# Kernel optimization log

Hardware: AMD Instinct MI355X
Metric: run time of the kernel (lower is better)

Reference implementation:

```python
import jax, jax.numpy as jnp
import numpy as np

NS_STEPS = 10
NS_A, NS_B, NS_C = 3.4445, -4.7750, 2.0315  # standard quintic Newton-Schulz coefficients
EPS = 1e-7

def orthogonalize(w):
    """Newton-Schulz iteration producing a (near-)orthogonal matrix from w."""
    din, dout = w.shape
    transpose = din > dout  # iterate on the wide orientation so X @ X.T is small
    x = w.T if transpose else w
    x = x / (jnp.linalg.norm(x) + EPS)  # spectral norm <= frobenius norm -> contraction

    def body(x, _):
        a = x @ x.T                      # (m, m) Gram matrix
        bmat = NS_B * a + NS_C * (a @ a)
        x = NS_A * x + bmat @ x
        return x, None

    x, _ = jax.lax.scan(body, x, None, length=NS_STEPS)
    return x.T if transpose else x


def setup_inputs() -> dict:
    key = jax.random.key(0)
    k1, k2, k3 = jax.random.split(key, 3)
    B, DIN, DOUT = 16384, 2048, 2048
    x = jax.random.normal(k1, (B, DIN), dtype=jnp.float32)
    w = jax.random.normal(k2, (DIN, DOUT), dtype=jnp.float32)
    b = jax.random.normal(k3, (DOUT,), dtype=jnp.float32) * 0.02
    return {"x": x, "w": w, "b": b}


def reference(x, w, b):
    w_orth = orthogonalize(w)
    return x @ w_orth + b
```

## Files before the change

### kernel.cpp

```cpp
#include <hip/hip_runtime.h>
#include <stdint.h>

typedef unsigned short u16;
typedef _Float16 half_t;
typedef __attribute__((ext_vector_type(4))) float f32x4;
typedef __attribute__((ext_vector_type(8))) _Float16 f16x8;

#define NS_A 3.4445f
#define NS_B -4.7750f
#define NS_C 2.0315f

#define SX      64.0f
#define INV_SX  (1.0f / 64.0f)
#define INV_SA  (1.0f / 4096.0f)

typedef const __attribute__((address_space(1))) void* as1_cvp;
typedef __attribute__((address_space(3))) void* as3_vp;
#define GLOAD_LDS16(gp, lp) \
    __builtin_amdgcn_global_load_lds((as1_cvp)(const void*)(gp), (as3_vp)(void*)(lp), 16, 0, 0)

template <int N> __device__ __forceinline__ void vmwait() {
    if constexpr (N == 0)       asm volatile("s_waitcnt vmcnt(0)" ::: "memory");
    else if constexpr (N == 4)  asm volatile("s_waitcnt vmcnt(4)" ::: "memory");
    else if constexpr (N == 6)  asm volatile("s_waitcnt vmcnt(6)" ::: "memory");
    else if constexpr (N == 8)  asm volatile("s_waitcnt vmcnt(8)" ::: "memory");
    else if constexpr (N == 12) asm volatile("s_waitcnt vmcnt(12)" ::: "memory");
    else static_assert(N == 0, "unsupported vmcnt");
}

template <int MODE>
__global__ __launch_bounds__(256, 2) void gemm_ns(
    const half_t* __restrict__ A, const half_t* __restrict__ B,
    const half_t* __restrict__ aux,
    void* __restrict__ outp, half_t* __restrict__ outpT,
    int M, int N, int K)
{
    __shared__ half_t As[3][64 * 64];
    __shared__ half_t Bs[3][128 * 64];
    const int tid  = threadIdx.x;
    const int wid  = tid >> 6;
    const int lane = tid & 63;
    const int wr = wid >> 1, wc = wid & 1;

    const int xcd = blockIdx.x & 7;
    const int ii  = blockIdx.x >> 3;
    const int brow = ((xcd & 1) * 16 + (ii >> 2)) * 64;
    const int bcol = ((xcd >> 1) * 4 + (ii & 3)) * 128;

    f32x4 acc[2][4] = {};

    const int r0   = tid >> 3;
    const int csrc = ((tid & 7) ^ ((tid >> 3) & 7)) * 8;
    const half_t* gA = A + (size_t)(brow + r0) * K + csrc;
    const half_t* gB = B + (size_t)(bcol + r0) * K + csrc;

    auto stage = [&](int slot, int kt) {
#pragma unroll
        for (int j = 0; j < 2; ++j)
            GLOAD_LDS16(gA + (size_t)(j * 32) * K + kt, &As[slot][(j * 256 + wid * 64) * 8]);
#pragma unroll
        for (int j = 0; j < 4; ++j)
            GLOAD_LDS16(gB + (size_t)(j * 32) * K + kt, &Bs[slot][(j * 256 + wid * 64) * 8]);
    };

    f16x8 af[2][2], bf[4][2];
    auto reads = [&](int slot) {
#pragma unroll
        for (int m = 0; m < 2; ++m) {
            const int row = wr * 32 + m * 16 + (lane & 15);
#pragma unroll
            for (int kk = 0; kk < 2; ++kk) {
                const int cc = (kk * 4 + (lane >> 4)) ^ (row & 7);
                af[m][kk] = *(const f16x8*)&As[slot][row * 64 + cc * 8];
            }
        }
#pragma unroll
        for (int n = 0; n < 4; ++n) {
            const int row = wc * 64 + n * 16 + (lane & 15);
#pragma unroll
            for (int kk = 0; kk < 2; ++kk) {
                const int cc = (kk * 4 + (lane >> 4)) ^ (row & 7);
                bf[n][kk] = *(const f16x8*)&Bs[slot][row * 64 + cc * 8];
            }
        }
    };
    auto mfma = [&]() {
        __builtin_amdgcn_s_setprio(1);
#pragma unroll
        for (int kk = 0; kk < 2; ++kk)
#pragma unroll
            for (int m = 0; m < 2; ++m)
#pragma unroll
                for (int n = 0; n < 4; ++n)
                    acc[m][n] = __builtin_amdgcn_mfma_f32_16x16x32_f16(af[m][kk], bf[n][kk], acc[m][n], 0, 0, 0);
        __builtin_amdgcn_s_setprio(0);
    };

    const int nsteps = K / 64;
    stage(0, 0);
    stage(1, 64);
    vmwait<6>();
    __builtin_amdgcn_s_barrier();

    int s = 0;
    for (; s < nsteps - 2; ++s) {
        reads(s % 3);
        stage((s + 2) % 3, (s + 2) * 64);
        vmwait<6>();
        __builtin_amdgcn_s_barrier();
        mfma();
        __builtin_amdgcn_s_barrier();
    }
    reads(s % 3);
    vmwait<0>();
    __builtin_amdgcn_s_barrier();
    mfma();
    __builtin_amdgcn_s_barrier();
    ++s;
    reads(s % 3);
    mfma();

#pragma unroll
    for (int m = 0; m < 2; ++m) {
#pragma unroll
        for (int n = 0; n < 4; ++n) {
            const int row0 = brow + wr * 32 + m * 16 + (lane >> 4) * 4;
            const int col  = bcol + wc * 64 + n * 16 + (lane & 15);
#pragma unroll
            for (int r = 0; r < 4; ++r) {
                const size_t idx = (size_t)(row0 + r) * N + col;
                const float v = acc[m][n][r];
                if (MODE == 0) {
                    ((half_t*)outp)[idx] = (half_t)v;
                } else if (MODE == 1) {
                    ((half_t*)outp)[idx] = (half_t)(NS_B * (float)aux[idx] + NS_C * v * INV_SA);
                } else {
                    const half_t o = (half_t)(NS_A * (float)aux[idx] + v * INV_SA);
                    ((half_t*)outp)[idx] = o;
                    if (outpT) outpT[(size_t)col * M + row0 + r] = o;
                }
            }
        }
    }
}

__global__ __launch_bounds__(512, 2) void gemm_fin(
    const half_t* __restrict__ A, const half_t* __restrict__ B,
    const float* __restrict__ bias, float* __restrict__ out,
    int M, int N, int K)
{
    __shared__ half_t As[4][256 * 32];
    __shared__ half_t Bs[4][256 * 32];
    const int tid  = threadIdx.x;
    const int wid  = tid >> 6;
    const int lane = tid & 63;
    const int wm = wid >> 2;
    const int wn = wid & 3;

    int bid = blockIdx.x;
    const int cpx = gridDim.x >> 3;
    bid = (bid & 7) * cpx + (bid >> 3);
    const int nbx  = N >> 8;
    const int brow = (bid / nbx) << 8;
    const int bcol = (bid % nbx) << 8;

    f32x4 acc[8][4] = {};

    const int r0   = tid >> 2;
    const int csrc = ((tid & 3) ^ ((tid >> 3) & 3)) * 8;
    const half_t* gA = A + (size_t)(brow + r0) * K + csrc;
    const half_t* gB = B + (size_t)(bcol + r0) * K + csrc;

    auto stage = [&](int slot, int kt) {
#pragma unroll
        for (int j = 0; j < 2; ++j)
            GLOAD_LDS16(gA + (size_t)(j * 128) * K + kt, &As[slot][(j * 512 + wid * 64) * 8]);
#pragma unroll
        for (int j = 0; j < 2; ++j)
            GLOAD_LDS16(gB + (size_t)(j * 128) * K + kt, &Bs[slot][(j * 512 + wid * 64) * 8]);
    };
    auto compute = [&](int slot) {
        f16x8 af[8], bf[4];
#pragma unroll
        for (int fr = 0; fr < 8; ++fr) {
            const int row = wm * 128 + fr * 16 + (lane & 15);
            af[fr] = *(const f16x8*)&As[slot][row * 32 + (((lane >> 4) ^ ((row >> 1) & 3)) * 8)];
        }
#pragma unroll
        for (int fc = 0; fc < 4; ++fc) {
            const int row = wn * 64 + fc * 16 + (lane & 15);
            bf[fc] = *(const f16x8*)&Bs[slot][row * 32 + (((lane >> 4) ^ ((row >> 1) & 3)) * 8)];
        }
        __builtin_amdgcn_s_setprio(1);
#pragma unroll
        for (int fr = 0; fr < 8; ++fr)
#pragma unroll
            for (int fc = 0; fc < 4; ++fc)
                acc[fr][fc] = __builtin_amdgcn_mfma_f32_16x16x32_f16(af[fr], bf[fc], acc[fr][fc], 0, 0, 0);
        __builtin_amdgcn_s_setprio(0);
    };

    stage(0, 0);
    stage(1, 32);
    stage(2, 64);
    int kt_next = 96;

#define RSTEP(SLOT, DOSTAGE, VMN) \
    do { \
        if (DOSTAGE) { stage((SLOT + 3) & 3, kt_next); kt_next += 32; } \
        vmwait<VMN>(); \
        __builtin_amdgcn_s_barrier(); \
        compute(SLOT); \
        __builtin_amdgcn_s_barrier(); \
    } while (0)

    const int nouter = ((K >> 5) - 4) >> 2;
    for (int tt = 0; tt < nouter; ++tt) {
        RSTEP(0, true, 12);
        RSTEP(1, true, 12);
        RSTEP(2, true, 12);
        RSTEP(3, true, 12);
    }
    RSTEP(0, true, 12);
    RSTEP(1, false, 8);
    RSTEP(2, false, 4);
    RSTEP(3, false, 0);
#undef RSTEP

#pragma unroll
    for (int fr = 0; fr < 8; ++fr) {
#pragma unroll
        for (int fc = 0; fc < 4; ++fc) {
            const int row0 = brow + wm * 128 + fr * 16 + (lane >> 4) * 4;
            const int col  = bcol + wn * 64 + fc * 16 + (lane & 15);
            const float bv = bias[col];
#pragma unroll
            for (int r = 0; r < 4; ++r)
                out[(size_t)(row0 + r) * N + col] = acc[fr][fc][r] * INV_SX + bv;
        }
    }
}

__global__ __launch_bounds__(256) void k_sumsq(const float* __restrict__ w,
                                               float* __restrict__ part, int n) {
    __shared__ float s[256];
    const int per  = n / 1024;
    const int base = blockIdx.x * per;
    float acc = 0.f;
    for (int i = threadIdx.x; i < per; i += 256) {
        float v = w[base + i];
        acc += v * v;
    }
    s[threadIdx.x] = acc;
    __syncthreads();
    for (int k = 128; k > 0; k >>= 1) {
        if (threadIdx.x < k) s[threadIdx.x] += s[threadIdx.x + k];
        __syncthreads();
    }
    if (threadIdx.x == 0) part[blockIdx.x] = s[0];
}

__global__ __launch_bounds__(256) void k_scalefin(const float* __restrict__ part,
                                                  float* __restrict__ scale) {
    __shared__ float s[256];
    float acc = 0.f;
    for (int i = threadIdx.x; i < 1024; i += 256) acc += part[i];
    s[threadIdx.x] = acc;
    __syncthreads();
    for (int k = 128; k > 0; k >>= 1) {
        if (threadIdx.x < k) s[threadIdx.x] += s[threadIdx.x + k];
        __syncthreads();
    }
    if (threadIdx.x == 0) scale[0] = SX / (sqrtf(s[0]) + 1e-7f);
}

__global__ __launch_bounds__(256) void k_scale_f16(const float* __restrict__ w,
                                                   const float* __restrict__ scale,
                                                   half_t* __restrict__ o, int n) {
    const int i = (blockIdx.x * 256 + threadIdx.x) * 4;
    if (i < n) {
        const float sc = scale[0];
        float4 v = *(const float4*)(w + i);
        o[i + 0] = (half_t)(v.x * sc);
        o[i + 1] = (half_t)(v.y * sc);
        o[i + 2] = (half_t)(v.z * sc);
        o[i + 3] = (half_t)(v.w * sc);
    }
}

__global__ __launch_bounds__(256) void k_cast_f16(const float* __restrict__ w,
                                                  half_t* __restrict__ o, int n) {
    const int i = (blockIdx.x * 256 + threadIdx.x) * 4;
    if (i < n) {
        float4 v = *(const float4*)(w + i);
        o[i + 0] = (half_t)v.x;
        o[i + 1] = (half_t)v.y;
        o[i + 2] = (half_t)v.z;
        o[i + 3] = (half_t)v.w;
    }
}

__global__ __launch_bounds__(256) void k_transpose(const u16* __restrict__ in,
                                                   u16* __restrict__ out, int n) {
    __shared__ u16 tile[64][65];
    const int bx = blockIdx.x * 64, by = blockIdx.y * 64;
    const int tx = threadIdx.x & 63, ty = threadIdx.x >> 6;
    for (int i = ty; i < 64; i += 4) tile[i][tx] = in[(size_t)(by + i) * n + bx + tx];
    __syncthreads();
    for (int i = ty; i < 64; i += 4) out[(size_t)(bx + i) * n + by + tx] = tile[tx][i];
}

extern "C" void kernel_launch(void* const* d_in, const int* in_sizes, int n_in,
                              void* d_out, int out_size, void* d_ws, size_t ws_size,
                              hipStream_t stream) {
    const float* x = (const float*)d_in[0];
    const float* w = (const float*)d_in[1];
    const float* b = (const float*)d_in[2];
    float* out = (float*)d_out;

    const int D  = 2048;
    const int Bm = in_sizes[0] / D;
    const int WN = D * D;
    const int XN = Bm * D;

    const size_t matB = (size_t)WN * 2;
    const bool pingpong = ws_size >= 8192 + 6 * matB + (size_t)XN * 2;

    char* ws = (char*)d_ws;
    float* part  = (float*)ws;
    float* scale = part + 1024;
    half_t* xb0  = (half_t*)(ws + 8192);
    half_t* xb1  = xb0 + WN;
    half_t* xbTa = xb1 + WN;
    half_t* xbTb = pingpong ? (xbTa + WN) : xbTa;
    half_t* amat = xbTb + WN;
    half_t* bmat = amat + WN;
    half_t* xinb = bmat + WN;

    k_sumsq<<<1024, 256, 0, stream>>>(w, part, WN);
    k_scalefin<<<1, 256, 0, stream>>>(part, scale);
    k_scale_f16<<<WN / 4 / 256, 256, 0, stream>>>(w, scale, xb0, WN);

    k_cast_f16<<<XN / 4 / 256, 256, 0, stream>>>(x, xinb, XN);

    const dim3 tgrid(D / 64, D / 64);
    k_transpose<<<tgrid, 256, 0, stream>>>((const u16*)xb0, (u16*)xbTa, D);

    const int ns_grid = (D / 64) * (D / 128);

    half_t* cur = xb0;
    half_t* nxt = xb1;
    half_t* Tr  = xbTa;
    half_t* Tw  = xbTb;
    for (int it = 0; it < 10; ++it) {
        gemm_ns<0><<<ns_grid, 256, 0, stream>>>(cur, cur, nullptr, amat, nullptr, D, D, D);
        gemm_ns<1><<<ns_grid, 256, 0, stream>>>(amat, amat, amat, bmat, nullptr, D, D, D);
        if (pingpong) {
            gemm_ns<2><<<ns_grid, 256, 0, stream>>>(bmat, Tr, cur, nxt, Tw, D, D, D);
            half_t* tt = Tr; Tr = Tw; Tw = tt;
        } else {
            gemm_ns<2><<<ns_grid, 256, 0, stream>>>(bmat, Tr, cur, nxt, nullptr, D, D, D);
            k_transpose<<<tgrid, 256, 0, stream>>>((const u16*)nxt, (u16*)Tr, D);
        }
        half_t* t = cur; cur = nxt; nxt = t;
    }

    const int fin_grid = (Bm / 256) * (D / 256);
    gemm_fin<<<fin_grid, 512, 0, stream>>>(xinb, Tr, b, out, Bm, D, D);
}
```

Before: 951.6 us.

## Exploit symmetry of Gram matrices with triangular-tile GEMM kernel

Result: no change. 963.9 us (+1.3%).

```diff
diff --git a/kernel.cpp b/kernel.cpp
--- a/kernel.cpp
+++ b/kernel.cpp
@@ -144,6 +144,121 @@
     }
 }
 
+template <int MODE>
+__global__ __launch_bounds__(256, 3) void gemm_sym(
+    const half_t* __restrict__ A, const half_t* __restrict__ aux,
+    half_t* __restrict__ outp, int N, int K)
+{
+    __shared__ half_t As[3][64 * 64];
+    __shared__ half_t Bs[3][64 * 64];
+    const int tid  = threadIdx.x;
+    const int wid  = tid >> 6;
+    const int lane = tid & 63;
+    const int wr = wid >> 1, wc = wid & 1;
+
+    const int bid = (blockIdx.x & 7) * 66 + (blockIdx.x >> 3);
+    int bi = (int)(32.5f - sqrtf(32.5f * 32.5f - 2.0f * (float)bid));
+    bi = bi < 0 ? 0 : (bi > 31 ? 31 : bi);
+    while (bi < 31 && (32 * (bi + 1) - ((bi + 1) * bi) / 2) <= bid) ++bi;
+    while (bi > 0 && (32 * bi - (bi * (bi - 1)) / 2) > bid) --bi;
+    const int bj = bi + (bid - (32 * bi - (bi * (bi - 1)) / 2));
+
+    const int brow = bi * 64;
+    const int bcol = bj * 64;
+
+    f32x4 acc[2][2] = {};
+
+    const int r0   = tid >> 3;
+    const int csrc = ((tid & 7) ^ ((tid >> 3) & 7)) * 8;
+    const half_t* gA = A + (size_t)(brow + r0) * K + csrc;
+    const half_t* gB = A + (size_t)(bcol + r0) * K + csrc;
+
+    auto stage = [&](int slot, int kt) {
+#pragma unroll
+        for (int j = 0; j < 2; ++j) {
+            GLOAD_LDS16(gA + (size_t)(j * 32) * K + kt, &As[slot][(j * 256 + wid * 64) * 8]);
+            GLOAD_LDS16(gB + (size_t)(j * 32) * K + kt, &Bs[slot][(j * 256 + wid * 64) * 8]);
+        }
+    };
+
+    f16x8 af[2][2], bf[2][2];
+    auto reads = [&](int slot) {
+#pragma unroll
+        for (int m = 0; m < 2; ++m) {
+            const int row = wr * 32 + m * 16 + (lane & 15);
+#pragma unroll
+            for (int kk = 0; kk < 2; ++kk) {
+                const int cc = (kk * 4 + (lane >> 4)) ^ (row & 7);
+                af[m][kk] = *(const f16x8*)&As[slot][row * 64 + cc * 8];
+            }
+        }
+#pragma unroll
+        for (int n = 0; n < 2; ++n) {
+            const int row = wc * 32 + n * 16 + (lane & 15);
+#pragma unroll
+            for (int kk = 0; kk < 2; ++kk) {
+                const int cc = (kk * 4 + (lane >> 4)) ^ (row & 7);
+                bf[n][kk] = *(const f16x8*)&Bs[slot][row * 64 + cc * 8];
+            }
+        }
+    };
+    auto mfma = [&]() {
+        __builtin_amdgcn_s_setprio(1);
+#pragma unroll
+        for (int kk = 0; kk < 2; ++kk)
+#pragma unroll
+            for (int m = 0; m < 2; ++m)
+#pragma unroll
+                for (int n = 0; n < 2; ++n)
+                    acc[m][n] = __builtin_amdgcn_mfma_f32_16x16x32_f16(af[m][kk], bf[n][kk], acc[m][n], 0, 0, 0);
+        __builtin_amdgcn_s_setprio(0);
+    };
+
+    const int nsteps = K / 64;
+    stage(0, 0);
+    stage(1, 64);
+    vmwait<4>();
+    __builtin_amdgcn_s_barrier();
+
+    int s = 0;
+    for (; s < nsteps - 2; ++s) {
+        reads(s % 3);
+        stage((s + 2) % 3, (s + 2) * 64);
+        vmwait<4>();
+        __builtin_amdgcn_s_barrier();
+        mfma();
+        __builtin_amdgcn_s_barrier();
+    }
+    reads(s % 3);
+    vmwait<0>();
+    __builtin_amdgcn_s_barrier();
+    mfma();
+    __builtin_amdgcn_s_barrier();
+    ++s;
+    reads(s % 3);
+    mfma();
+
+#pragma unroll
+    for (int m = 0; m < 2; ++m) {
+#pragma unroll
+        for (int n = 0; n < 2; ++n) {
+            const int row0 = brow + wr * 32 + m * 16 + (lane >> 4) * 4;
+            const int col  = bcol + wc * 32 + n * 16 + (lane & 15);
+#pragma unroll
+            for (int r = 0; r < 4; ++r) {
+                const int row = row0 + r;
+                const size_t idx = (size_t)row * N + col;
+                const float v = acc[m][n][r];
+                half_t o;
+                if (MODE == 0) o = (half_t)v;
+                else           o = (half_t)(NS_B * (float)aux[idx] + NS_C * v * INV_SA);
+                if (row <= col) outp[idx] = o;
+                if (row < col)  outp[(size_t)col * N + row] = o;
+            }
+        }
+    }
+}
+
 __global__ __launch_bounds__(512, 2) void gemm_fin(
     const half_t* __restrict__ A, const half_t* __restrict__ B,
     const float* __restrict__ bias, float* __restrict__ out,
@@ -346,15 +461,16 @@
     const dim3 tgrid(D / 64, D / 64);
     k_transpose<<<tgrid, 256, 0, stream>>>((const u16*)xb0, (u16*)xbTa, D);
 
-    const int ns_grid = (D / 64) * (D / 128);
+    const int ns_grid  = (D / 64) * (D / 128);
+    const int sym_grid = (D / 64) * (D / 64 + 1) / 2;
 
     half_t* cur = xb0;
     half_t* nxt = xb1;
     half_t* Tr  = xbTa;
     half_t* Tw  = xbTb;
     for (int it = 0; it < 10; ++it) {
-        gemm_ns<0><<<ns_grid, 256, 0, stream>>>(cur, cur, nullptr, amat, nullptr, D, D, D);
-        gemm_ns<1><<<ns_grid, 256, 0, stream>>>(amat, amat, amat, bmat, nullptr, D, D, D);
+        gemm_sym<0><<<sym_grid, 256, 0, stream>>>(cur, nullptr, amat, D, D);
+        gemm_sym<1><<<sym_grid, 256, 0, stream>>>(amat, amat, bmat, D, D);
         if (pingpong) {
             gemm_ns<2><<<ns_grid, 256, 0, stream>>>(bmat, Tr, cur, nxt, Tw, D, D, D);
             half_t* tt = Tr; Tr = Tw; Tw = tt;
```

## Switch final GEMM to double-buffered LDS pipeline and raise occupancy hint

Applied to the files above, without the earlier changes.

After: 2.171 ms. 128% more time.

```diff
diff --git a/kernel.cpp b/kernel.cpp
--- a/kernel.cpp
+++ b/kernel.cpp
@@ -144,13 +144,13 @@
     }
 }
 
-__global__ __launch_bounds__(512, 2) void gemm_fin(
+__global__ __launch_bounds__(512, 4) void gemm_fin(
     const half_t* __restrict__ A, const half_t* __restrict__ B,
     const float* __restrict__ bias, float* __restrict__ out,
     int M, int N, int K)
 {
-    __shared__ half_t As[4][256 * 32];
-    __shared__ half_t Bs[4][256 * 32];
+    __shared__ half_t As[2][256 * 32];
+    __shared__ half_t Bs[2][256 * 32];
     const int tid  = threadIdx.x;
     const int wid  = tid >> 6;
     const int lane = tid & 63;
@@ -200,32 +200,20 @@
         __builtin_amdgcn_s_setprio(0);
     };
 
+    const int nsteps = K >> 5;
     stage(0, 0);
-    stage(1, 32);
-    stage(2, 64);
-    int kt_next = 96;
-
-#define RSTEP(SLOT, DOSTAGE, VMN) \
-    do { \
-        if (DOSTAGE) { stage((SLOT + 3) & 3, kt_next); kt_next += 32; } \
-        vmwait<VMN>(); \
-        __builtin_amdgcn_s_barrier(); \
-        compute(SLOT); \
-        __builtin_amdgcn_s_barrier(); \
-    } while (0)
-
-    const int nouter = ((K >> 5) - 4) >> 2;
-    for (int tt = 0; tt < nouter; ++tt) {
-        RSTEP(0, true, 12);
-        RSTEP(1, true, 12);
-        RSTEP(2, true, 12);
-        RSTEP(3, true, 12);
-    }
-    RSTEP(0, true, 12);
-    RSTEP(1, false, 8);
-    RSTEP(2, false, 4);
-    RSTEP(3, false, 0);
-#undef RSTEP
+    vmwait<0>();
+    __builtin_amdgcn_s_barrier();
+
+    for (int s = 0; s < nsteps; ++s) {
+        const int slot = s & 1;
+        if (s + 1 < nsteps) stage(slot ^ 1, (s + 1) * 32);
+        compute(slot);
+        if (s + 1 < nsteps) {
+            vmwait<0>();
+            __builtin_amdgcn_s_barrier();
+        }
+    }
 
 #pragma unroll
     for (int fr = 0; fr < 8; ++fr) {
```

## Switch NS GEMM to double-buffered pipeline, fuse scale+transpose, skip dead final store

Applied to the files above, without the earlier changes.

Result: slower. 1.162 ms (+22.1%).

```diff
diff --git a/kernel.cpp b/kernel.cpp
--- a/kernel.cpp
+++ b/kernel.cpp
@@ -22,21 +22,20 @@
 template <int N> __device__ __forceinline__ void vmwait() {
     if constexpr (N == 0)       asm volatile("s_waitcnt vmcnt(0)" ::: "memory");
     else if constexpr (N == 4)  asm volatile("s_waitcnt vmcnt(4)" ::: "memory");
-    else if constexpr (N == 6)  asm volatile("s_waitcnt vmcnt(6)" ::: "memory");
     else if constexpr (N == 8)  asm volatile("s_waitcnt vmcnt(8)" ::: "memory");
     else if constexpr (N == 12) asm volatile("s_waitcnt vmcnt(12)" ::: "memory");
     else static_assert(N == 0, "unsupported vmcnt");
 }
 
 template <int MODE>
-__global__ __launch_bounds__(256, 2) void gemm_ns(
+__global__ __launch_bounds__(256, 3) void gemm_ns(
     const half_t* __restrict__ A, const half_t* __restrict__ B,
     const half_t* __restrict__ aux,
     void* __restrict__ outp, half_t* __restrict__ outpT,
     int M, int N, int K)
 {
-    __shared__ half_t As[3][64 * 64];
-    __shared__ half_t Bs[3][128 * 64];
+    __shared__ half_t As[2][64 * 64];
+    __shared__ half_t Bs[2][128 * 64];
     const int tid  = threadIdx.x;
     const int wid  = tid >> 6;
     const int lane = tid & 63;
@@ -98,27 +97,19 @@
 
     const int nsteps = K / 64;
     stage(0, 0);
-    stage(1, 64);
-    vmwait<6>();
-    __builtin_amdgcn_s_barrier();
-
-    int s = 0;
-    for (; s < nsteps - 2; ++s) {
-        reads(s % 3);
-        stage((s + 2) % 3, (s + 2) * 64);
-        vmwait<6>();
-        __builtin_amdgcn_s_barrier();
-        mfma();
-        __builtin_amdgcn_s_barrier();
-    }
-    reads(s % 3);
     vmwait<0>();
     __builtin_amdgcn_s_barrier();
-    mfma();
-    __builtin_amdgcn_s_barrier();
-    ++s;
-    reads(s % 3);
-    mfma();
+
+    for (int s = 0; s < nsteps; ++s) {
+        const int slot = s & 1;
+        if (s + 1 < nsteps) stage(slot ^ 1, (s + 1) * 64);
+        reads(slot);
+        mfma();
+        if (s + 1 < nsteps) {
+            vmwait<0>();
+            __builtin_amdgcn_s_barrier();
+        }
+    }
 
 #pragma unroll
     for (int m = 0; m < 2; ++m) {
@@ -136,7 +127,7 @@
                     ((half_t*)outp)[idx] = (half_t)(NS_B * (float)aux[idx] + NS_C * v * INV_SA);
                 } else {
                     const half_t o = (half_t)(NS_A * (float)aux[idx] + v * INV_SA);
-                    ((half_t*)outp)[idx] = o;
+                    if (outp)  ((half_t*)outp)[idx] = o;
                     if (outpT) outpT[(size_t)col * M + row0 + r] = o;
                 }
             }
@@ -274,18 +265,23 @@
     if (threadIdx.x == 0) scale[0] = SX / (sqrtf(s[0]) + 1e-7f);
 }
 
-__global__ __launch_bounds__(256) void k_scale_f16(const float* __restrict__ w,
-                                                   const float* __restrict__ scale,
-                                                   half_t* __restrict__ o, int n) {
-    const int i = (blockIdx.x * 256 + threadIdx.x) * 4;
-    if (i < n) {
-        const float sc = scale[0];
-        float4 v = *(const float4*)(w + i);
-        o[i + 0] = (half_t)(v.x * sc);
-        o[i + 1] = (half_t)(v.y * sc);
-        o[i + 2] = (half_t)(v.z * sc);
-        o[i + 3] = (half_t)(v.w * sc);
-    }
+__global__ __launch_bounds__(256) void k_scale_tr(const float* __restrict__ w,
+                                                  const float* __restrict__ scale,
+                                                  u16* __restrict__ o,
+                                                  u16* __restrict__ oT, int n) {
+    __shared__ u16 tile[64][65];
+    const int bx = blockIdx.x * 64, by = blockIdx.y * 64;
+    const int tx = threadIdx.x & 63, ty = threadIdx.x >> 6;
+    const float sc = scale[0];
+    for (int i = ty; i < 64; i += 4) {
+        const half_t h = (half_t)(w[(size_t)(by + i) * n + bx + tx] * sc);
+        const u16 u = __builtin_bit_cast(u16, h);
+        o[(size_t)(by + i) * n + bx + tx] = u;
+        tile[i][tx] = u;
+    }
+    __syncthreads();
+    for (int i = ty; i < 64; i += 4)
+        oT[(size_t)(bx + i) * n + by + tx] = tile[tx][i];
 }
 
 __global__ __launch_bounds__(256) void k_cast_f16(const float* __restrict__ w,
@@ -339,12 +335,10 @@
 
     k_sumsq<<<1024, 256, 0, stream>>>(w, part, WN);
     k_scalefin<<<1, 256, 0, stream>>>(part, scale);
-    k_scale_f16<<<WN / 4 / 256, 256, 0, stream>>>(w, scale, xb0, WN);
+    const dim3 tgrid(D / 64, D / 64);
+    k_scale_tr<<<tgrid, 256, 0, stream>>>(w, scale, (u16*)xb0, (u16*)xbTa, D);
 
     k_cast_f16<<<XN / 4 / 256, 256, 0, stream>>>(x, xinb, XN);
-
-    const dim3 tgrid(D / 64, D / 64);
-    k_transpose<<<tgrid, 256, 0, stream>>>((const u16*)xb0, (u16*)xbTa, D);
 
     const int ns_grid = (D / 64) * (D / 128);
 
@@ -356,7 +350,8 @@
         gemm_ns<0><<<ns_grid, 256, 0, stream>>>(cur, cur, nullptr, amat, nullptr, D, D, D);
         gemm_ns<1><<<ns_grid, 256, 0, stream>>>(amat, amat, amat, bmat, nullptr, D, D, D);
         if (pingpong) {
-            gemm_ns<2><<<ns_grid, 256, 0, stream>>>(bmat, Tr, cur, nxt, Tw, D, D, D);
+            half_t* outp = (it == 9) ? nullptr : nxt;
+            gemm_ns<2><<<ns_grid, 256, 0, stream>>>(bmat, Tr, cur, outp, Tw, D, D, D);
             half_t* tt = Tr; Tr = Tw; Tw = tt;
         } else {
             gemm_ns<2><<<ns_grid, 256, 0, stream>>>(bmat, Tr, cur, nxt, nullptr, D, D, D);
```
